# Kernel tuning notes

Measured on AMD Instinct MI355X. Metric: run time of the kernel, lower is better.

Reference implementation:

```python
import jax, jax.numpy as jnp
import numpy as np

B, SEQ, NVAR, DM, K = 2, 512, 64, 128, 2
SCALE = DM ** -0.5  # ScaledDotProductAttention scale, lsa=False so constant


def _period_branch(x4, Wel, bel, Wq, bq, Wk, bk, Wv, bv, Wo, bo, period):
    # x4: [B, DM(time), NVAR, DM(dim)] -- output of start_embed
    pad = (-DM) % period
    pn = (DM + pad) // period  # period_num
    xp = jnp.pad(x4, ((0, 0), (0, pad), (0, 0), (0, 0)))
    # torch .unfold(dim=1, size=period, step=period) -> [B, pn, NVAR, DM, period]
    xw = xp.reshape(B, pn, period, NVAR, DM).transpose(0, 1, 3, 4, 2)
    # emb_linear over the d_model (dim) axis
    xw = jnp.einsum('bqndl,ed->bqnel', xw, Wel) + bel[None, None, None, :, None]
    # -> [B, NVAR, dim, pn, period] then flatten to conv1d layout [bn, dim, L]
    X = xw.transpose(0, 2, 3, 1, 4).reshape(B * NVAR, DM, pn * period)
    # 1x1 Conv1d QKV projections over the channel (dim) axis
    q = jnp.einsum('bdl,ed->bel', X, Wq) + bq[None, :, None]
    k = jnp.einsum('bdl,ed->bel', X, Wk) + bk[None, :, None]
    v = jnp.einsum('bdl,ed->bel', X, Wv) + bv[None, :, None]
    q_s = q.reshape(B * NVAR, DM, pn, period).transpose(0, 1, 3, 2)  # [bn,dim,pl,pn]
    k_s = k.reshape(B * NVAR, DM, pn, period)                         # [bn,dim,pn,pl]
    v_s = v.reshape(B * NVAR, DM, pn, period).transpose(0, 1, 3, 2)  # [bn,dim,pl,pn]
    attn = jax.nn.softmax(jnp.einsum('bdip,bdpj->bdij', q_s, k_s) * SCALE, axis=-1)
    o = jnp.einsum('bdij,bdjp->bdip', attn, v_s)  # [bn, dim, period, pn]
    o = o.reshape(B * NVAR, DM, period * pn)[:, :, :DM]  # truncate to n_heads=DM
    return o @ Wo.T + bo  # to_out Linear(n_heads, n_heads), dropout eval-mode


def reference(x, W_emb, b_emb, W_start, b_start, Wel, bel, Wq, bq, Wk, bk, Wv, bv, Wo, bo, f1, f2):
    # inverted embedding: Linear(seq_len->d_model) over time, then permute -> [B, DM, NVAR]
    xe = (jnp.einsum('bsn,sd->bnd', x, W_emb) + b_emb).transpose(0, 2, 1)
    # FFT_for_Period amplitudes; top-k frequency indices f1,f2 are static (host-side in torch)
    amp = jnp.abs(jnp.fft.rfft(xe, axis=1)).mean(-1)  # [B, DM//2+1]
    pw = jax.nn.softmax(jnp.stack([amp[:, f1], amp[:, f2]], -1), axis=-1)  # [B, K]
    # start_embed: Linear(1 -> d_model) -> [B, DM, NVAR, DM]
    x4 = xe[..., None] * W_start + b_start
    outs = [_period_branch(x4, Wel, bel, Wq, bq, Wk, bk, Wv, bv, Wo, bo, DM // f)
            for f in (f1, f2)]
    res = jnp.stack(outs, -1)                      # [B*NVAR, DM, DM, K]
    pw_b = jnp.repeat(pw, NVAR, axis=0)            # [B*NVAR, K] (b-major order matches reshape)
    out = (res * pw_b[:, None, None, :]).sum(-1)
    return out.reshape(B, NVAR, DM, DM)


def setup_inputs() -> dict:
    key = jax.random.key(0)
    ks = jax.random.split(key, 16)
    s = 0.02
    d = {
        'x': jax.random.normal(ks[0], (B, SEQ, NVAR), jnp.float32),
        'W_emb': jax.random.normal(ks[1], (SEQ, DM), jnp.float32) * s,
        'b_emb': jax.random.normal(ks[2], (DM,), jnp.float32) * s,
        'W_start': jax.random.normal(ks[3], (DM,), jnp.float32) * s,
        'b_start': jax.random.normal(ks[4], (DM,), jnp.float32) * s,
        'Wel': jax.random.normal(ks[5], (DM, DM), jnp.float32) * s,
        'bel': jax.random.normal(ks[6], (DM,), jnp.float32) * s,
        'Wq': jax.random.normal(ks[7], (DM, DM), jnp.float32) * s,
        'bq': jax.random.normal(ks[8], (DM,), jnp.float32) * s,
        'Wk': jax.random.normal(ks[9], (DM, DM), jnp.float32) * s,
        'bk': jax.random.normal(ks[10], (DM,), jnp.float32) * s,
        'Wv': jax.random.normal(ks[11], (DM, DM), jnp.float32) * s,
        'bv': jax.random.normal(ks[12], (DM,), jnp.float32) * s,
        'Wo': jax.random.normal(ks[13], (DM, DM), jnp.float32) * s,
        'bo': jax.random.normal(ks[14], (DM,), jnp.float32) * s,
    }
    # host-side FFT period detection, mirroring torch's .detach().cpu().numpy() topk
    xe = np.einsum('bsn,sd->bnd', np.asarray(d['x']), np.asarray(d['W_emb'])) + np.asarray(d['b_emb'])
    xe = xe.transpose(0, 2, 1)  # [B, DM, NVAR]
    fl = np.abs(np.fft.rfft(xe, axis=1)).mean(0).mean(-1)
    fl[0] = 0.0
    top = np.argsort(-fl, kind='stable')[:K]
    d['f1'] = int(top[0])
    d['f2'] = int(top[1])
    return d
```

## Files before the change

### kernel.cpp

```cpp
#include <hip/hip_runtime.h>

#define DMD 128
#define NV 64
#define BB 2
#define SQ 512
#define NBN 128
#define ASCALE 0.08838834764831845f
#define L2E 1.4426950408889634f
#define CSC (ASCALE * L2E)

#define WS_XE  0
#define WS_VEC (WS_XE + NBN*DMD)
#define WS_OB  (WS_VEC + 9*DMD)
#define WS_AMP (WS_OB + NBN*DMD*DMD)

__global__ __launch_bounds__(512) void k_xe(const float* __restrict__ x,
                                            const float* __restrict__ W_emb,
                                            const float* __restrict__ b_emb,
                                            const int* __restrict__ f1p,
                                            const int* __restrict__ f2p,
                                            const float* __restrict__ Wel, const float* __restrict__ bel,
                                            const float* __restrict__ W_start, const float* __restrict__ b_start,
                                            const float* __restrict__ Wq, const float* __restrict__ bq,
                                            const float* __restrict__ Wk, const float* __restrict__ bk,
                                            const float* __restrict__ Wv, const float* __restrict__ bv,
                                            float* __restrict__ ws) {
    int blk = blockIdx.x;
    int tid = threadIdx.x;
    __shared__ __align__(16) float4 xsh[SQ];
    __shared__ float part[3][DMD][4];
    __shared__ float red[2][16];
    __shared__ __align__(16) float A[DMD], C[DMD], BL[DMD];

    if (blk < 32) {
        int b = blk >> 4, n0 = (blk & 15) * 4;
        int t = tid & 127, sc = tid >> 7;
        xsh[tid] = *reinterpret_cast<const float4*>(&x[(b * SQ + tid) * NV + n0]);
        __syncthreads();
        float a0 = 0.f, a1 = 0.f, a2 = 0.f, a3 = 0.f;
        const float* W = W_emb + (sc * 128) * DMD + t;
#pragma unroll 8
        for (int s = 0; s < 128; ++s) {
            float w = W[s * DMD];
            float4 xv = xsh[sc * 128 + s];
            a0 = fmaf(xv.x, w, a0); a1 = fmaf(xv.y, w, a1);
            a2 = fmaf(xv.z, w, a2); a3 = fmaf(xv.w, w, a3);
        }
        if (sc) {
            part[sc - 1][t][0] = a0; part[sc - 1][t][1] = a1;
            part[sc - 1][t][2] = a2; part[sc - 1][t][3] = a3;
        }
        __syncthreads();
        if (sc == 0) {
            float be = b_emb[t];
            float r0 = a0 + part[0][t][0] + part[1][t][0] + part[2][t][0] + be;
            float r1 = a1 + part[0][t][1] + part[1][t][1] + part[2][t][1] + be;
            float r2 = a2 + part[0][t][2] + part[1][t][2] + part[2][t][2] + be;
            float r3 = a3 + part[0][t][3] + part[1][t][3] + part[2][t][3] + be;
            ws[WS_XE + (b * NV + n0 + 0) * DMD + t] = r0;
            ws[WS_XE + (b * NV + n0 + 1) * DMD + t] = r1;
            ws[WS_XE + (b * NV + n0 + 2) * DMD + t] = r2;
            ws[WS_XE + (b * NV + n0 + 3) * DMD + t] = r3;
            int f1v = f1p[0], f2v = f2p[0];
            float angA = (float)((f1v * t) & 127) * 0.04908738521234052f;
            float angB = (float)((f2v * t) & 127) * 0.04908738521234052f;
            float cA = cosf(angA), sA = sinf(angA);
            float cB = cosf(angB), sB = sinf(angB);
            float vals[16] = { r0*cA, r0*sA, r0*cB, r0*sB,
                               r1*cA, r1*sA, r1*cB, r1*sB,
                               r2*cA, r2*sA, r2*cB, r2*sB,
                               r3*cA, r3*sA, r3*cB, r3*sB };
#pragma unroll
            for (int k = 0; k < 16; ++k) {
                float v = vals[k];
                v += __shfl_xor(v, 1);  v += __shfl_xor(v, 2);
                v += __shfl_xor(v, 4);  v += __shfl_xor(v, 8);
                v += __shfl_xor(v, 16); v += __shfl_xor(v, 32);
                vals[k] = v;
            }
            if ((tid & 63) == 0) {
                int w = tid >> 6;
#pragma unroll
                for (int k = 0; k < 16; ++k) red[w][k] = vals[k];
            }
        }
        __syncthreads();
        if (tid < 8) {
            int nl = tid >> 1, fs = tid & 1;
            int base = nl * 4 + fs * 2;
            float re = red[0][base] + red[1][base];
            float im = red[0][base + 1] + red[1][base + 1];
            ws[WS_AMP + (b * NV + n0 + nl) * 2 + fs] = sqrtf(re * re + im * im);
        }
    } else {
        int e = tid;
        if (tid < 128) {
            float a = 0.f, c = 0.f;
            const float4* We4 = reinterpret_cast<const float4*>(Wel + e * DMD);
            const float4* Ws4 = reinterpret_cast<const float4*>(W_start);
            const float4* Bs4 = reinterpret_cast<const float4*>(b_start);
#pragma unroll 8
            for (int d4 = 0; d4 < 32; ++d4) {
                float4 w = We4[d4], s4 = Ws4[d4], t4 = Bs4[d4];
                a = fmaf(w.x, s4.x, fmaf(w.y, s4.y, fmaf(w.z, s4.z, fmaf(w.w, s4.w, a))));
                c = fmaf(w.x, t4.x, fmaf(w.y, t4.y, fmaf(w.z, t4.z, fmaf(w.w, t4.w, c))));
            }
            A[e] = a;
            C[e] = c + bel[e];
            BL[e] = bel[e];
        }
        __syncthreads();
        if (tid < 128) {
            float aq = 0, cq = 0, pq = 0, ak = 0, ck = 0, pk = 0, av = 0, cv = 0, pv = 0;
            const float4* Wq4 = reinterpret_cast<const float4*>(Wq + e * DMD);
            const float4* Wk4 = reinterpret_cast<const float4*>(Wk + e * DMD);
            const float4* Wv4 = reinterpret_cast<const float4*>(Wv + e * DMD);
            const float4* A4 = reinterpret_cast<const float4*>(A);
            const float4* C4 = reinterpret_cast<const float4*>(C);
            const float4* B4 = reinterpret_cast<const float4*>(BL);
#pragma unroll 4
            for (int d4 = 0; d4 < 32; ++d4) {
                float4 Ad = A4[d4], Cd = C4[d4], Bd = B4[d4];
                float4 wq = Wq4[d4], wk = Wk4[d4], wv = Wv4[d4];
                aq = fmaf(wq.x, Ad.x, fmaf(wq.y, Ad.y, fmaf(wq.z, Ad.z, fmaf(wq.w, Ad.w, aq))));
                cq = fmaf(wq.x, Cd.x, fmaf(wq.y, Cd.y, fmaf(wq.z, Cd.z, fmaf(wq.w, Cd.w, cq))));
                pq = fmaf(wq.x, Bd.x, fmaf(wq.y, Bd.y, fmaf(wq.z, Bd.z, fmaf(wq.w, Bd.w, pq))));
                ak = fmaf(wk.x, Ad.x, fmaf(wk.y, Ad.y, fmaf(wk.z, Ad.z, fmaf(wk.w, Ad.w, ak))));
                ck = fmaf(wk.x, Cd.x, fmaf(wk.y, Cd.y, fmaf(wk.z, Cd.z, fmaf(wk.w, Cd.w, ck))));
                pk = fmaf(wk.x, Bd.x, fmaf(wk.y, Bd.y, fmaf(wk.z, Bd.z, fmaf(wk.w, Bd.w, pk))));
                av = fmaf(wv.x, Ad.x, fmaf(wv.y, Ad.y, fmaf(wv.z, Ad.z, fmaf(wv.w, Ad.w, av))));
                cv = fmaf(wv.x, Cd.x, fmaf(wv.y, Cd.y, fmaf(wv.z, Cd.z, fmaf(wv.w, Cd.w, cv))));
                pv = fmaf(wv.x, Bd.x, fmaf(wv.y, Bd.y, fmaf(wv.z, Bd.z, fmaf(wv.w, Bd.w, pv))));
            }
            float* V = ws + WS_VEC;
            V[0 * DMD + e] = aq; V[1 * DMD + e] = cq + bq[e]; V[2 * DMD + e] = pq + bq[e];
            V[3 * DMD + e] = ak; V[4 * DMD + e] = ck + bk[e]; V[5 * DMD + e] = pk + bk[e];
            V[6 * DMD + e] = av; V[7 * DMD + e] = cv + bv[e]; V[8 * DMD + e] = pv + bv[e];
        }
    }
}


__device__ __forceinline__ void attn_rank1(float pwv, const float (*Vsh)[4],
                                           const float* xs, float* __restrict__ ob,
                                           int rowbase, int tid) {
    float xi = xs[tid];
    float t[4], l[4], ax[4];
#pragma unroll
    for (int k = 0; k < 4; ++k) {
        float Aq = Vsh[0][k], Cq = Vsh[1][k], Ak = Vsh[3][k];
        t[k] = CSC * fmaf(xi, Aq, Cq) * Ak;
        l[k] = 0.f; ax[k] = 0.f;
    }
#pragma unroll 4
    for (int j = 0; j < DMD; ++j) {
        float xj = xs[j];
#pragma unroll
        for (int k = 0; k < 4; ++k) {
            float ev = exp2f(t[k] * xj);
            l[k] += ev;
            ax[k] = fmaf(ev, xj, ax[k]);
        }
    }
#pragma unroll
    for (int k = 0; k < 4; ++k) {
        float Av = Vsh[6][k], Cv = Vsh[7][k];
        float o = fmaf(Av, ax[k] / l[k], Cv);
        ob[rowbase + k * DMD + tid] = pwv * o;
    }
}

template<int PP, int NP, int EB>
__device__ __forceinline__ void attn_pow2(float pwv, const float (*Vsh)[4],
                                          const float* xs, float* __restrict__ ob,
                                          int rowbase, int tid) {
    const int UH = PP / 4;
    int lane4 = tid & 3, i0 = tid >> 2, jb = lane4 * UH;

    float xq[NP][UH], U2[UH];
#pragma unroll
    for (int u = 0; u < UH; ++u) {
        int j = jb + u;
        float s = 0.f;
#pragma unroll
        for (int q = 0; q < NP; ++q) { float xv = xs[q * PP + j]; xq[q][u] = xv; s += xv; }
        U2[u] = s;
    }
    const int NREP = (PP == 64) ? 2 : 1;
#pragma unroll
    for (int rep = 0; rep < NREP; ++rep) {
        int i = i0 + rep * 32;
        float G2[UH];
#pragma unroll
        for (int u = 0; u < UH; ++u) G2[u] = 0.f;
#pragma unroll
        for (int q = 0; q < NP; ++q) {
            float xi = xs[q * PP + i];
#pragma unroll
            for (int u = 0; u < UH; ++u) G2[u] = fmaf(xi, xq[q][u], G2[u]);
        }
#pragma unroll
        for (int eg = 0; eg < 4; eg += EB) {
            float d1[EB], d2[EB], l[EB];
            float accq[NP][EB];
#pragma unroll
            for (int k = 0; k < EB; ++k) {
                float t = CSC * Vsh[3][eg + k];
                d1[k] = t * Vsh[0][eg + k];
                d2[k] = t * Vsh[1][eg + k];
                l[k] = 0.f;
#pragma unroll
                for (int q = 0; q < NP; ++q) accq[q][k] = 0.f;
            }
#pragma unroll
            for (int u = 0; u < UH; ++u) {
                float gg = G2[u], uu = U2[u];
                float ev[EB];
#pragma unroll
                for (int k = 0; k < EB; ++k) ev[k] = exp2f(fmaf(d1[k], gg, d2[k] * uu));
#pragma unroll
                for (int k = 0; k < EB; ++k) {
                    l[k] += ev[k];
#pragma unroll
                    for (int q = 0; q < NP; ++q) accq[q][k] = fmaf(ev[k], xq[q][u], accq[q][k]);
                }
            }
#pragma unroll
            for (int k = 0; k < EB; ++k) { l[k] += __shfl_xor(l[k], 1); l[k] += __shfl_xor(l[k], 2); }
#pragma unroll
            for (int q = 0; q < NP; ++q)
#pragma unroll
                for (int k = 0; k < EB; ++k) {
                    accq[q][k] += __shfl_xor(accq[q][k], 1);
                    accq[q][k] += __shfl_xor(accq[q][k], 2);
                }
            if (lane4 == 0) {
#pragma unroll
                for (int k = 0; k < EB; ++k) {
                    float li = 1.f / l[k];
                    float Av = Vsh[6][eg + k], Cv = Vsh[7][eg + k];
#pragma unroll
                    for (int q = 0; q < NP; ++q) {
                        float o = fmaf(Av, accq[q][k] * li, Cv);
                        ob[rowbase + (eg + k) * DMD + i * NP + q] = pwv * o;
                    }
                }
            }
        }
    }
}

template<int UB>
__device__ __forceinline__ void attn_small(
    int P, int pn, int r, int Prows, float pwv,
    const float (*Vsh)[4], const float* xs, const float* U, const float* xt,
    float* W, float* __restrict__ ob, int rowbase, int tid)
{
    int GP = P + 1;
    int tot = Prows * P;
    unsigned mP = (4096u + (unsigned)P - 1u) / (unsigned)P;
    unsigned mpn = (4096u + (unsigned)pn - 1u) / (unsigned)pn;

    bool v0 = (tid < tot);
    int i0 = (int)(((unsigned)tid * mP) >> 12);
    int j0 = tid - i0 * P;
    bool A0 = (i0 < r), c0 = (j0 < r);
    float xtj0 = xt[j0], Uj0 = U[j0];
    float xti0 = A0 ? xt[i0] : 0.f;
    float g0 = 0.f;
    for (int p = 0; p < pn - 1; ++p) g0 = fmaf(xs[p * P + i0], xs[p * P + j0], g0);
    float Gx0 = (A0 && c0) ? fmaf(xti0, xtj0, g0) : g0;
    float Ux0 = (A0 && c0) ? Uj0 + xtj0 : Uj0;
    float Xw0 = (!A0 && c0) ? xtj0 : 0.f;
    float mw0 = c0 ? 1.f : 0.f;
    int wa0 = i0 * GP + j0;

    int idx1 = tid + 128;
    bool v1 = (idx1 < tot);
    int idx1c = v1 ? idx1 : 0;
    int i1 = (int)(((unsigned)idx1c * mP) >> 12);
    int j1 = idx1c - i1 * P;
    bool A1 = (i1 < r), c1 = (j1 < r);
    float xtj1 = xt[j1], Uj1 = U[j1];
    float xti1 = A1 ? xt[i1] : 0.f;
    float g1 = 0.f;
    for (int p = 0; p < pn - 1; ++p) g1 = fmaf(xs[p * P + i1], xs[p * P + j1], g1);
    float Gx1 = (A1 && c1) ? fmaf(xti1, xtj1, g1) : g1;
    float Ux1 = (A1 && c1) ? Uj1 + xtj1 : Uj1;
    float Xw1 = (!A1 && c1) ? xtj1 : 0.f;
    float mw1 = c1 ? 1.f : 0.f;
    int wa1 = i1 * GP + j1;

    int i2 = (int)(((unsigned)tid * mpn) >> 12);
    int p2 = tid - i2 * pn;
    bool lastp = (p2 == pn - 1);
    int row2 = i2 * GP;
    float xsr[UB];
#pragma unroll
    for (int j = 0; j < UB; ++j) {
        int idx = p2 * P + j;
        xsr[j] = (j < P && idx < DMD) ? xs[idx] : 0.f;
    }

    float s[4][2];
#pragma unroll
    for (int ec = 0; ec < 4; ++ec) {
        float Aq = Vsh[0][ec], Cq = Vsh[1][ec], Pq = Vsh[2][ec];
        float Ak = Vsh[3][ec], Ck = Vsh[4][ec], Pk = Vsh[5][ec];
        float t = CSC * Ak;
        float d1 = t * Aq, d2 = t * Cq, d3 = t * Pq;
        float ckpk = CSC * (Ck - Pk);
        float aS0 = A0 ? fmaf(Aq, xti0, Cq) : Pq;
        s[ec][0] = fmaf(d1, Gx0, fmaf(d2, Ux0, fmaf(d3, Xw0, (ckpk * aS0) * mw0)));
        float aS1 = A1 ? fmaf(Aq, xti1, Cq) : Pq;
        s[ec][1] = fmaf(d1, Gx1, fmaf(d2, Ux1, fmaf(d3, Xw1, (ckpk * aS1) * mw1)));
    }
#pragma unroll
    for (int ec = 0; ec < 4; ++ec) { s[ec][0] = exp2f(s[ec][0]); s[ec][1] = exp2f(s[ec][1]); }
#pragma unroll
    for (int ec = 0; ec < 4; ++ec) {
        if (v0) W[ec * 288 + wa0] = s[ec][0];
        if (v1) W[ec * 288 + wa1] = s[ec][1];
    }
    __syncthreads();

#pragma unroll
    for (int ec = 0; ec < 4; ++ec) {
        float Av = Vsh[6][ec], Cv = Vsh[7][ec], Pv = Vsh[8][ec];
        float l = 0.f, wr = 0.f, ax = 0.f;
#pragma unroll
        for (int j = 0; j < UB; ++j) {
            float w = W[ec * 288 + row2 + ((j < P) ? j : 0)];
            w = (j < P) ? w : 0.f;
            l += w;
            wr += (j < r) ? w : 0.f;
            ax = fmaf(w, xsr[j], ax);
        }
        float li = 1.f / l;
        float o;
        if (lastp) { float sl = wr * li; o = fmaf(Av, ax * li, fmaf(Cv, sl, Pv * (1.f - sl))); }
        else       o = fmaf(Av, ax * li, Cv);
        ob[rowbase + ec * DMD + tid] = pwv * o;
    }
}

template<int UH, int NP>
__device__ __forceinline__ void attn_midA(
    int P, int pn, int r, int Prows, float pwv,
    const float (*Vsh)[4], const float* xs, const float* U,
    const float* xt, float* __restrict__ ob, int rowbase, int tid)
{
    int lane4 = tid & 3;
    int i0 = tid >> 2;
    int jb = lane4 * UH;

    float Ur[UH], xtr[UH], xq0[UH], xq1[UH];
#pragma unroll
    for (int u = 0; u < UH; ++u) {
        int j = jb + u, jc = (j < P) ? j : 0;
        Ur[u] = U[jc];
        xtr[u] = xt[jc];
        xq0[u] = (j < DMD) ? xs[j] : 0.f;
        int i1x = P + j;
        xq1[u] = (i1x < DMD) ? xs[i1x] : 0.f;
    }
    int nrep = (Prows > 32) ? 2 : 1;
    for (int rep = 0; rep < nrep; ++rep) {
        int i = i0 + rep * 32;
        bool rowact = (i < Prows);
        int ic = rowact ? i : 0;
        float xtic = xt[ic];
        bool rowvalid = (ic < r);
        float g[UH];
#pragma unroll
        for (int u = 0; u < UH; ++u) g[u] = 0.f;
        for (int p = 0; p < pn - 1; ++p) {
            float xi = xs[p * P + ic];
#pragma unroll
            for (int u = 0; u < UH; ++u) {
                int j = jb + u, jc = (j < P) ? j : 0;
                g[u] = fmaf(xi, xs[p * P + jc], g[u]);
            }
        }
        for (int ec = 0; ec < 4; ++ec) {
            float Aq = Vsh[0][ec], Cq = Vsh[1][ec], Pq = Vsh[2][ec];
            float Ak = Vsh[3][ec], Ck = Vsh[4][ec], Pk = Vsh[5][ec];
            float Av = Vsh[6][ec], Cv = Vsh[7][ec], Pv = Vsh[8][ec];
            float c1 = CSC * Aq * Ak, c3 = CSC * Cq * Ak;
            float asi = CSC * (rowvalid ? fmaf(xtic, Aq, Cq) : Pq);

            float l0 = 0.f, l1 = 0.f, w0 = 0.f, w1 = 0.f;
            float accq[NP];
#pragma unroll
            for (int q = 0; q < NP; ++q) accq[q] = 0.f;
#pragma unroll
            for (int u = 0; u < UH; ++u) {
                int j = jb + u;
                float bK = (j < r) ? fmaf(xtr[u], Ak, Ck) : Pk;
                float S = fmaf(asi, bK, fmaf(c3, Ur[u], c1 * g[u]));
                float ev = exp2f(S);
                ev = (j < P) ? ev : 0.f;
                if (u & 1) l1 += ev; else l0 += ev;
                float evr = (j < r) ? ev : 0.f;
                if (u & 1) w1 += evr; else w0 += evr;
                accq[0] = fmaf(ev, xq0[u], accq[0]);
                if (NP >= 2) accq[1] = fmaf(ev, xq1[u], accq[1]);
#pragma unroll
                for (int q = 2; q < NP; ++q) {
                    int idx = q * P + j;
                    float xv = (idx < DMD) ? xs[idx] : 0.f;
                    accq[q] = fmaf(ev, xv, accq[q]);
                }
            }
            float l = l0 + l1, wr = w0 + w1;
            l += __shfl_xor(l, 1);  l += __shfl_xor(l, 2);
            wr += __shfl_xor(wr, 1); wr += __shfl_xor(wr, 2);
#pragma unroll
            for (int q = 0; q < NP; ++q) {
                if (q < pn) {
                    accq[q] += __shfl_xor(accq[q], 1);
                    accq[q] += __shfl_xor(accq[q], 2);
                }
            }
            if (lane4 == 0 && rowact) {
                float li = 1.f / l;
#pragma unroll
                for (int q = 0; q < NP; ++q) {
                    if (q < pn) {
                        int mo = i * pn + q;
                        if (mo < DMD) {
                            float o;
                            if (q == pn - 1) {
                                float sl = wr * li;
                                o = fmaf(Av, accq[q] * li, fmaf(Cv, sl, Pv * (1.f - sl)));
                            } else {
                                o = fmaf(Av, accq[q] * li, Cv);
                            }
                            ob[rowbase + ec * DMD + mo] = pwv * o;
                        }
                    }
                }
            }
        }
    }
}

__global__ __launch_bounds__(128) void k_attn(const int* __restrict__ f1p,
                                              const int* __restrict__ f2p,
                                              float* __restrict__ ws,
                                              float* __restrict__ outb) {
    int bn = blockIdx.y, b = bn >> 6;
    int e0 = blockIdx.x * 4;
    int br = blockIdx.z;
    int tid = threadIdx.x;

    __shared__ float xs[DMD], U[64], xt[64];
    __shared__ float Vsh[9][4];
    __shared__ float W[4 * 288];
    __shared__ float pwsh[2];

    xs[tid] = ws[WS_XE + bn * DMD + tid];
    if (tid < 36) Vsh[tid >> 2][tid & 3] = ws[WS_VEC + (tid >> 2) * DMD + e0 + (tid & 3)];
    if (tid < 64) {
        float a0 = ws[WS_AMP + (b * NV + tid) * 2 + 0];
        float a1 = ws[WS_AMP + (b * NV + tid) * 2 + 1];
#pragma unroll
        for (int off = 32; off > 0; off >>= 1) {
            a0 += __shfl_down(a0, off);
            a1 += __shfl_down(a1, off);
        }
        if (tid == 0) {
            a0 *= (1.0f / NV); a1 *= (1.0f / NV);
            float m = fmaxf(a0, a1);
            float e0v = expf(a0 - m), e1v = expf(a1 - m);
            float inv = 1.0f / (e0v + e1v);
            pwsh[0] = e0v * inv;
            pwsh[1] = e1v * inv;
        }
    }
    int f = br ? f2p[0] : f1p[0];
    float* ob = br ? outb : (ws + WS_OB);
    int rowbase = (bn * DMD + e0) * DMD;
    __syncthreads();
    float pwv = pwsh[br];

    int P = DMD / f;
    int pn = (DMD + P - 1) / P;
    int r = DMD - (pn - 1) * P;
    int Prows = (DMD + pn - 1) / pn;

    if (P == DMD) {
        attn_rank1(pwv, Vsh, xs, ob, rowbase, tid);
        return;
    }
    if (tid < P) {
        float s = 0.f;
        for (int p = 0; p < pn - 1; ++p) s += xs[p * P + tid];
        U[tid] = s;
        xt[tid] = (tid < r) ? xs[(pn - 1) * P + tid] : 0.f;
    }
    __syncthreads();

    if (P <= 4)       attn_small<4>(P, pn, r, Prows, pwv, Vsh, xs, U, xt, W, ob, rowbase, tid);
    else if (P <= 8)  attn_small<8>(P, pn, r, Prows, pwv, Vsh, xs, U, xt, W, ob, rowbase, tid);
    else if (P <= 16) attn_small<16>(P, pn, r, Prows, pwv, Vsh, xs, U, xt, W, ob, rowbase, tid);
    else if (P == 64) attn_pow2<64, 2, 2>(pwv, Vsh, xs, ob, rowbase, tid);
    else if (P == 32) attn_pow2<32, 4, 4>(pwv, Vsh, xs, ob, rowbase, tid);
    else if (P > 32)  attn_midA<16, 4>(P, pn, r, Prows, pwv, Vsh, xs, U, xt, ob, rowbase, tid);
    else              attn_midA<8, 8>(P, pn, r, Prows, pwv, Vsh, xs, U, xt, ob, rowbase, tid);
}

__global__ __launch_bounds__(256) void k_out(const float* __restrict__ Wo,
                                             const float* __restrict__ bo,
                                             const float* __restrict__ ws,
                                             float* __restrict__ out) {
    int blk = blockIdx.x;
    int bn0 = (blk >> 2) * 2;
    int e0  = (blk & 3) * 32;
    int tid = threadIdx.x;
    __shared__ __align__(16) float WTc[32 * 132];
    __shared__ __align__(16) float oT[2][32][36];
    int hg = tid & 31, eg = tid >> 5, h0 = hg * 4;

    float acc[2][4][4];
#pragma unroll
    for (int a = 0; a < 2; ++a)
#pragma unroll
        for (int c = 0; c < 4; ++c)
#pragma unroll
            for (int d = 0; d < 4; ++d) acc[a][c][d] = 0.f;

    for (int mc = 0; mc < 4; ++mc) {
        int m0 = mc * 32;
        __syncthreads();
        for (int idx = tid; idx < 4096; idx += 256) {
            int h = idx >> 5, mm = idx & 31;
            WTc[mm * 132 + h] = Wo[h * DMD + m0 + mm];
        }
        for (int idx = tid; idx < 2048; idx += 256) {
            int bnl = idx >> 10, rem = idx & 1023, e = rem >> 5, mm = rem & 31;
            int gi = ((bn0 + bnl) * DMD + e0 + e) * DMD + m0 + mm;
            oT[bnl][mm][e] = ws[WS_OB + gi] + out[gi];
        }
        __syncthreads();
#pragma unroll 4
        for (int mm = 0; mm < 32; ++mm) {
            const float4 wv = *reinterpret_cast<const float4*>(&WTc[mm * 132 + h0]);
            const float4 q0 = *reinterpret_cast<const float4*>(&oT[0][mm][eg * 4]);
            const float4 q1 = *reinterpret_cast<const float4*>(&oT[1][mm][eg * 4]);
            float ae[2][4] = {{q0.x, q0.y, q0.z, q0.w}, {q1.x, q1.y, q1.z, q1.w}};
#pragma unroll
            for (int bnl = 0; bnl < 2; ++bnl) {
#pragma unroll
                for (int el = 0; el < 4; ++el) {
                    float a = ae[bnl][el];
                    acc[bnl][el][0] = fmaf(a, wv.x, acc[bnl][el][0]);
                    acc[bnl][el][1] = fmaf(a, wv.y, acc[bnl][el][1]);
                    acc[bnl][el][2] = fmaf(a, wv.z, acc[bnl][el][2]);
                    acc[bnl][el][3] = fmaf(a, wv.w, acc[bnl][el][3]);
                }
            }
        }
    }
    const float4 bov = *reinterpret_cast<const float4*>(&bo[h0]);
#pragma unroll
    for (int bnl = 0; bnl < 2; ++bnl) {
#pragma unroll
        for (int el = 0; el < 4; ++el) {
            float4 res = { acc[bnl][el][0] + bov.x, acc[bnl][el][1] + bov.y,
                           acc[bnl][el][2] + bov.z, acc[bnl][el][3] + bov.w };
            int e = e0 + eg * 4 + el;
            *reinterpret_cast<float4*>(&out[((bn0 + bnl) * DMD + e) * DMD + h0]) = res;
        }
    }
}

extern "C" void kernel_launch(void* const* d_in, const int* in_sizes, int n_in,
                              void* d_out, int out_size, void* d_ws, size_t ws_size,
                              hipStream_t stream) {
    const float* x       = (const float*)d_in[0];
    const float* W_emb   = (const float*)d_in[1];
    const float* b_emb   = (const float*)d_in[2];
    const float* W_start = (const float*)d_in[3];
    const float* b_start = (const float*)d_in[4];
    const float* Wel     = (const float*)d_in[5];
    const float* bel     = (const float*)d_in[6];
    const float* Wq      = (const float*)d_in[7];
    const float* bq      = (const float*)d_in[8];
    const float* Wk      = (const float*)d_in[9];
    const float* bk      = (const float*)d_in[10];
    const float* Wv      = (const float*)d_in[11];
    const float* bv      = (const float*)d_in[12];
    const float* Wo      = (const float*)d_in[13];
    const float* bo      = (const float*)d_in[14];
    const int*   f1p     = (const int*)d_in[15];
    const int*   f2p     = (const int*)d_in[16];
    float* ws  = (float*)d_ws;
    float* out = (float*)d_out;

    k_xe<<<33, 512, 0, stream>>>(x, W_emb, b_emb, f1p, f2p,
                                 Wel, bel, W_start, b_start,
                                 Wq, bq, Wk, bk, Wv, bv, ws);
    k_attn<<<dim3(32, NBN, 2), 128, 0, stream>>>(f1p, f2p, ws, out);
    k_out<<<256, 256, 0, stream>>>(Wo, bo, ws, out);
}
```

Before: 85.22 us.

## Spread embedding over more blocks and defer period weighting to output kernel

The embedding kernel now uses one block per (batch, variable) instead of one block per four variables, so 128 blocks run instead of 32. Each block drops the float4 gather from x and the 16-way shuffle reduction. The softmax period-weight computation moves out of the attention kernel, which now writes unweighted outputs, into the output projection kernel. There the weights are applied when the two branch outputs are combined. This removes a per-block softmax preamble from the 8192 attention blocks but adds it to the 256 output blocks, and gives up reuse of the W_emb loads across four variables.

```diff
diff --git a/kernel.cpp b/kernel.cpp
--- a/kernel.cpp
+++ b/kernel.cpp
@@ -27,70 +27,46 @@
                                             float* __restrict__ ws) {
     int blk = blockIdx.x;
     int tid = threadIdx.x;
-    __shared__ __align__(16) float4 xsh[SQ];
-    __shared__ float part[3][DMD][4];
-    __shared__ float red[2][16];
+    __shared__ float xsh[SQ];
+    __shared__ float part[3][DMD];
+    __shared__ float red[2][4];
     __shared__ __align__(16) float A[DMD], C[DMD], BL[DMD];
 
-    if (blk < 32) {
-        int b = blk >> 4, n0 = (blk & 15) * 4;
+    if (blk < NBN) {
+        int bn = blk, b = bn >> 6, n = bn & 63;
         int t = tid & 127, sc = tid >> 7;
-        xsh[tid] = *reinterpret_cast<const float4*>(&x[(b * SQ + tid) * NV + n0]);
+        xsh[tid] = x[(b * SQ + tid) * NV + n];
         __syncthreads();
-        float a0 = 0.f, a1 = 0.f, a2 = 0.f, a3 = 0.f;
+        float acc = 0.f;
         const float* W = W_emb + (sc * 128) * DMD + t;
 #pragma unroll 8
-        for (int s = 0; s < 128; ++s) {
-            float w = W[s * DMD];
-            float4 xv = xsh[sc * 128 + s];
-            a0 = fmaf(xv.x, w, a0); a1 = fmaf(xv.y, w, a1);
-            a2 = fmaf(xv.z, w, a2); a3 = fmaf(xv.w, w, a3);
-        }
-        if (sc) {
-            part[sc - 1][t][0] = a0; part[sc - 1][t][1] = a1;
-            part[sc - 1][t][2] = a2; part[sc - 1][t][3] = a3;
-        }
+        for (int s = 0; s < 128; ++s) acc = fmaf(xsh[sc * 128 + s], W[s * DMD], acc);
+        if (sc) part[sc - 1][t] = acc;
         __syncthreads();
         if (sc == 0) {
-            float be = b_emb[t];
-            float r0 = a0 + part[0][t][0] + part[1][t][0] + part[2][t][0] + be;
-            float r1 = a1 + part[0][t][1] + part[1][t][1] + part[2][t][1] + be;
-            float r2 = a2 + part[0][t][2] + part[1][t][2] + part[2][t][2] + be;
-            float r3 = a3 + part[0][t][3] + part[1][t][3] + part[2][t][3] + be;
-            ws[WS_XE + (b * NV + n0 + 0) * DMD + t] = r0;
-            ws[WS_XE + (b * NV + n0 + 1) * DMD + t] = r1;
-            ws[WS_XE + (b * NV + n0 + 2) * DMD + t] = r2;
-            ws[WS_XE + (b * NV + n0 + 3) * DMD + t] = r3;
+            float r = acc + part[0][t] + part[1][t] + part[2][t] + b_emb[t];
+            ws[WS_XE + bn * DMD + t] = r;
             int f1v = f1p[0], f2v = f2p[0];
             float angA = (float)((f1v * t) & 127) * 0.04908738521234052f;
             float angB = (float)((f2v * t) & 127) * 0.04908738521234052f;
-            float cA = cosf(angA), sA = sinf(angA);
-            float cB = cosf(angB), sB = sinf(angB);
-            float vals[16] = { r0*cA, r0*sA, r0*cB, r0*sB,
-                               r1*cA, r1*sA, r1*cB, r1*sB,
-                               r2*cA, r2*sA, r2*cB, r2*sB,
-                               r3*cA, r3*sA, r3*cB, r3*sB };
-#pragma unroll
-            for (int k = 0; k < 16; ++k) {
-                float v = vals[k];
-                v += __shfl_xor(v, 1);  v += __shfl_xor(v, 2);
-                v += __shfl_xor(v, 4);  v += __shfl_xor(v, 8);
-                v += __shfl_xor(v, 16); v += __shfl_xor(v, 32);
-                vals[k] = v;
+            float v0 = r * cosf(angA), v1 = r * sinf(angA);
+            float v2 = r * cosf(angB), v3 = r * sinf(angB);
+#pragma unroll
+            for (int off = 32; off > 0; off >>= 1) {
+                v0 += __shfl_xor(v0, off); v1 += __shfl_xor(v1, off);
+                v2 += __shfl_xor(v2, off); v3 += __shfl_xor(v3, off);
             }
             if ((tid & 63) == 0) {
                 int w = tid >> 6;
-#pragma unroll
-                for (int k = 0; k < 16; ++k) red[w][k] = vals[k];
+                red[w][0] = v0; red[w][1] = v1; red[w][2] = v2; red[w][3] = v3;
             }
         }
         __syncthreads();
-        if (tid < 8) {
-            int nl = tid >> 1, fs = tid & 1;
-            int base = nl * 4 + fs * 2;
-            float re = red[0][base] + red[1][base];
-            float im = red[0][base + 1] + red[1][base + 1];
-            ws[WS_AMP + (b * NV + n0 + nl) * 2 + fs] = sqrtf(re * re + im * im);
+        if (tid == 0) {
+            float re0 = red[0][0] + red[1][0], im0 = red[0][1] + red[1][1];
+            float re1 = red[0][2] + red[1][2], im1 = red[0][3] + red[1][3];
+            ws[WS_AMP + bn * 2 + 0] = sqrtf(re0 * re0 + im0 * im0);
+            ws[WS_AMP + bn * 2 + 1] = sqrtf(re1 * re1 + im1 * im1);
         }
     } else {
         int e = tid;
@@ -141,7 +117,7 @@
 }
 
 
-__device__ __forceinline__ void attn_rank1(float pwv, const float (*Vsh)[4],
+__device__ __forceinline__ void attn_rank1(const float (*Vsh)[4],
                                            const float* xs, float* __restrict__ ob,
                                            int rowbase, int tid) {
     float xi = xs[tid];
@@ -165,13 +141,12 @@
 #pragma unroll
     for (int k = 0; k < 4; ++k) {
         float Av = Vsh[6][k], Cv = Vsh[7][k];
-        float o = fmaf(Av, ax[k] / l[k], Cv);
-        ob[rowbase + k * DMD + tid] = pwv * o;
+        ob[rowbase + k * DMD + tid] = fmaf(Av, ax[k] / l[k], Cv);
     }
 }
 
 template<int PP, int NP, int EB>
-__device__ __forceinline__ void attn_pow2(float pwv, const float (*Vsh)[4],
+__device__ __forceinline__ void attn_pow2(const float (*Vsh)[4],
                                           const float* xs, float* __restrict__ ob,
                                           int rowbase, int tid) {
     const int UH = PP / 4;
@@ -241,8 +216,7 @@
                     float Av = Vsh[6][eg + k], Cv = Vsh[7][eg + k];
 #pragma unroll
                     for (int q = 0; q < NP; ++q) {
-                        float o = fmaf(Av, accq[q][k] * li, Cv);
-                        ob[rowbase + (eg + k) * DMD + i * NP + q] = pwv * o;
+                        ob[rowbase + (eg + k) * DMD + i * NP + q] = fmaf(Av, accq[q][k] * li, Cv);
                     }
                 }
             }
@@ -252,7 +226,7 @@
 
 template<int UB>
 __device__ __forceinline__ void attn_small(
-    int P, int pn, int r, int Prows, float pwv,
+    int P, int pn, int r, int Prows,
     const float (*Vsh)[4], const float* xs, const float* U, const float* xt,
     float* W, float* __restrict__ ob, int rowbase, int tid)
 {
@@ -340,13 +314,13 @@
         float o;
         if (lastp) { float sl = wr * li; o = fmaf(Av, ax * li, fmaf(Cv, sl, Pv * (1.f - sl))); }
         else       o = fmaf(Av, ax * li, Cv);
-        ob[rowbase + ec * DMD + tid] = pwv * o;
+        ob[rowbase + ec * DMD + tid] = o;
     }
 }
 
 template<int UH, int NP>
 __device__ __forceinline__ void attn_midA(
-    int P, int pn, int r, int Prows, float pwv,
+    int P, int pn, int r, int Prows,
     const float (*Vsh)[4], const float* xs, const float* U,
     const float* xt, float* __restrict__ ob, int rowbase, int tid)
 {
@@ -436,7 +410,7 @@
                             } else {
                                 o = fmaf(Av, accq[q] * li, Cv);
                             }
-                            ob[rowbase + ec * DMD + mo] = pwv * o;
+                            ob[rowbase + ec * DMD + mo] = o;
                         }
                     }
                 }
@@ -449,7 +423,7 @@
                                               const int* __restrict__ f2p,
                                               float* __restrict__ ws,
                                               float* __restrict__ outb) {
-    int bn = blockIdx.y, b = bn >> 6;
+    int bn = blockIdx.y;
     int e0 = blockIdx.x * 4;
     int br = blockIdx.z;
     int tid = threadIdx.x;
@@ -457,10 +431,54 @@
     __shared__ float xs[DMD], U[64], xt[64];
     __shared__ float Vsh[9][4];
     __shared__ float W[4 * 288];
-    __shared__ float pwsh[2];
 
     xs[tid] = ws[WS_XE + bn * DMD + tid];
     if (tid < 36) Vsh[tid >> 2][tid & 3] = ws[WS_VEC + (tid >> 2) * DMD + e0 + (tid & 3)];
+    int f = br ? f2p[0] : f1p[0];
+    float* ob = br ? outb : (ws + WS_OB);
+    int rowbase = (bn * DMD + e0) * DMD;
+    __syncthreads();
+
+    int P = DMD / f;
+    int pn = (DMD + P - 1) / P;
+    int r = DMD - (pn - 1) * P;
+    int Prows = (DMD + pn - 1) / pn;
+
+    if (P == DMD) {
+        attn_rank1(Vsh, xs, ob, rowbase, tid);
+        return;
+    }
+    if (tid < P) {
+        float s = 0.f;
+        for (int p = 0; p < pn - 1; ++p) s += xs[p * P + tid];
+        U[tid] = s;
+        xt[tid] = (tid < r) ? xs[(pn - 1) * P + tid] : 0.f;
+    }
+    __syncthreads();
+
+    if (P <= 4)       attn_small<4>(P, pn, r, Prows, Vsh, xs, U, xt, W, ob, rowbase, tid);
+    else if (P <= 8)  attn_small<8>(P, pn, r, Prows, Vsh, xs, U, xt, W, ob, rowbase, tid);
+    else if (P <= 16) attn_small<16>(P, pn, r, Prows, Vsh, xs, U, xt, W, ob, rowbase, tid);
+    else if (P == 64) attn_pow2<64, 2, 2>(Vsh, xs, ob, rowbase, tid);
+    else if (P == 32) attn_pow2<32, 4, 4>(Vsh, xs, ob, rowbase, tid);
+    else if (P > 32)  attn_midA<16, 4>(P, pn, r, Prows, Vsh, xs, U, xt, ob, rowbase, tid);
+    else              attn_midA<8, 8>(P, pn, r, Prows, Vsh, xs, U, xt, ob, rowbase, tid);
+}
+
+__global__ __launch_bounds__(256) void k_out(const float* __restrict__ Wo,
+                                             const float* __restrict__ bo,
+                                             const float* __restrict__ ws,
+                                             float* __restrict__ out) {
+    int blk = blockIdx.x;
+    int bn0 = (blk >> 2) * 2;
+    int e0  = (blk & 3) * 32;
+    int b = bn0 >> 6;
+    int tid = threadIdx.x;
+    __shared__ __align__(16) float WTc[32 * 132];
+    __shared__ __align__(16) float oT[2][32][36];
+    __shared__ float pwsh[2];
+    int hg = tid & 31, eg = tid >> 5, h0 = hg * 4;
+
     if (tid < 64) {
         float a0 = ws[WS_AMP + (b * NV + tid) * 2 + 0];
         float a1 = ws[WS_AMP + (b * NV + tid) * 2 + 1];
@@ -478,49 +496,8 @@
             pwsh[1] = e1v * inv;
         }
     }
-    int f = br ? f2p[0] : f1p[0];
-    float* ob = br ? outb : (ws + WS_OB);
-    int rowbase = (bn * DMD + e0) * DMD;
     __syncthreads();
-    float pwv = pwsh[br];
-
-    int P = DMD / f;
-    int pn = (DMD + P - 1) / P;
-    int r = DMD - (pn - 1) * P;
-    int Prows = (DMD + pn - 1) / pn;
-
-    if (P == DMD) {
-        attn_rank1(pwv, Vsh, xs, ob, rowbase, tid);
-        return;
-    }
-    if (tid < P) {
-        float s = 0.f;
-        for (int p = 0; p < pn - 1; ++p) s += xs[p * P + tid];
-        U[tid] = s;
-        xt[tid] = (tid < r) ? xs[(pn - 1) * P + tid] : 0.f;
-    }
-    __syncthreads();
-
-    if (P <= 4)       attn_small<4>(P, pn, r, Prows, pwv, Vsh, xs, U, xt, W, ob, rowbase, tid);
-    else if (P <= 8)  attn_small<8>(P, pn, r, Prows, pwv, Vsh, xs, U, xt, W, ob, rowbase, tid);
-    else if (P <= 16) attn_small<16>(P, pn, r, Prows, pwv, Vsh, xs, U, xt, W, ob, rowbase, tid);
-    else if (P == 64) attn_pow2<64, 2, 2>(pwv, Vsh, xs, ob, rowbase, tid);
-    else if (P == 32) attn_pow2<32, 4, 4>(pwv, Vsh, xs, ob, rowbase, tid);
-    else if (P > 32)  attn_midA<16, 4>(P, pn, r, Prows, pwv, Vsh, xs, U, xt, ob, rowbase, tid);
-    else              attn_midA<8, 8>(P, pn, r, Prows, pwv, Vsh, xs, U, xt, ob, rowbase, tid);
-}
-
-__global__ __launch_bounds__(256) void k_out(const float* __restrict__ Wo,
-                                             const float* __restrict__ bo,
-                                             const float* __restrict__ ws,
-                                             float* __restrict__ out) {
-    int blk = blockIdx.x;
-    int bn0 = (blk >> 2) * 2;
-    int e0  = (blk & 3) * 32;
-    int tid = threadIdx.x;
-    __shared__ __align__(16) float WTc[32 * 132];
-    __shared__ __align__(16) float oT[2][32][36];
-    int hg = tid & 31, eg = tid >> 5, h0 = hg * 4;
+    float pw0 = pwsh[0], pw1 = pwsh[1];
 
     float acc[2][4][4];
 #pragma unroll
@@ -540,7 +517,7 @@
         for (int idx = tid; idx < 2048; idx += 256) {
             int bnl = idx >> 10, rem = idx & 1023, e = rem >> 5, mm = rem & 31;
             int gi = ((bn0 + bnl) * DMD + e0 + e) * DMD + m0 + mm;
-            oT[bnl][mm][e] = ws[WS_OB + gi] + out[gi];
+            oT[bnl][mm][e] = fmaf(pw0, ws[WS_OB + gi], pw1 * out[gi]);
         }
         __syncthreads();
 #pragma unroll 4
@@ -598,9 +575,9 @@
     float* ws  = (float*)d_ws;
     float* out = (float*)d_out;
 
-    k_xe<<<33, 512, 0, stream>>>(x, W_emb, b_emb, f1p, f2p,
-                                 Wel, bel, W_start, b_start,
-                                 Wq, bq, Wk, bk, Wv, bv, ws);
+    k_xe<<<NBN + 1, 512, 0, stream>>>(x, W_emb, b_emb, f1p, f2p,
+                                      Wel, bel, W_start, b_start,
+                                      Wq, bq, Wk, bk, Wv, bv, ws);
     k_attn<<<dim3(32, NBN, 2), 128, 0, stream>>>(f1p, f2p, ws, out);
     k_out<<<256, 256, 0, stream>>>(Wo, bo, ws, out);
 }
```

Result: faster. 81.01 us (-4.9%).
